# Kernel optimization log

Hardware: AMD Instinct MI355X
Metric: run time of the kernel (lower is better)

## Reference

```python
import jax, jax.numpy as jnp
import numpy as np

K = 3  # kernel_size per dim
DIM = 3
NUM_K = K ** DIM  # 27
# the 2^3 corner offsets of the linear B-spline support
OFFS = np.array([[(s >> d) & 1 for d in range(DIM)] for s in range(2 ** DIM)], dtype=np.int32)  # [8,3]
STRIDES = np.array([K ** d for d in range(DIM)], dtype=np.int32)  # [1,3,9]


def bspline_basis(pseudo):
    """Open B-spline basis, degree 1. pseudo: [E,3] in [0,1]. Returns basis [E,8], kidx [E,8]."""
    v = pseudo * (K - 1)
    i0 = jnp.clip(jnp.floor(v), 0, K - 2)
    f = v - i0  # fractional part in [0,1]
    i0 = i0.astype(jnp.int32)
    offs = jnp.asarray(OFFS)  # [8,3]
    w = jnp.where(offs[None].astype(bool), f[:, None, :], 1.0 - f[:, None, :])  # [E,8,3]
    basis = jnp.prod(w, axis=-1)  # [E,8]
    kidx = jnp.sum((i0[:, None, :] + offs[None]) * jnp.asarray(STRIDES)[None, None, :], axis=-1)  # [E,8]
    return basis, kidx


def spline_conv(x, src, dst, pseudo, W, Wroot, b, num_nodes):
    """SplineConv (degree 1, mean aggregation, root weight + bias)."""
    cout = W.shape[-1]
    xW = jnp.einsum('nc,kco->nko', x, W)  # [N,27,Cout]
    basis, kidx = bspline_basis(pseudo)
    flat = src[:, None] * NUM_K + kidx  # [E,8]
    g = xW.reshape(-1, cout)[flat]  # [E,8,Cout] -- dominant gather
    msg = jnp.einsum('es,eso->eo', basis, g)  # [E,Cout]
    agg = jax.ops.segment_sum(msg, dst, num_segments=num_nodes)
    cnt = jax.ops.segment_sum(jnp.ones((src.shape[0],), x.dtype), dst, num_segments=num_nodes)
    return agg / jnp.maximum(cnt, 1.0)[:, None] + x @ Wroot + b


def seg_max(x, seg, num_segments):
    m = jax.ops.segment_max(x, seg, num_segments=num_segments)
    return jnp.where(jnp.isfinite(m), m, 0.0)  # empty clusters -> 0


def setup_inputs() -> dict:
    key = jax.random.key(0)
    ks = jax.random.split(key, 16)
    N, E, B = 80000, 1280000, 16
    N1, N2 = N // 2, N1 if False else (N // 2) // 2  # N1=40000, N2=20000
    N1 = N // 2
    N2 = N1 // 2
    x = jax.random.normal(ks[0], (N, 2), dtype=jnp.float32)
    edge_index = jax.random.randint(ks[1], (2, E), 0, N, dtype=jnp.int32)
    edge_attr = jax.random.uniform(ks[2], (E, 3), dtype=jnp.float32)
    batch = jnp.sort(jax.random.randint(ks[3], (N,), 0, B, dtype=jnp.int32))
    cluster1 = jax.random.randint(ks[4], (N,), 0, N1, dtype=jnp.int32)
    cluster2 = jax.random.randint(ks[5], (N1,), 0, N2, dtype=jnp.int32)
    W1 = jax.random.normal(ks[6], (NUM_K, 2, 8), dtype=jnp.float32) * 0.3
    root1 = jax.random.normal(ks[7], (2, 8), dtype=jnp.float32) * 0.3
    b1 = jnp.zeros((8,), jnp.float32)
    W2 = jax.random.normal(ks[8], (NUM_K, 8, 16), dtype=jnp.float32) * 0.2
    root2 = jax.random.normal(ks[9], (8, 16), dtype=jnp.float32) * 0.2
    b2 = jnp.zeros((16,), jnp.float32)
    fc1_w = jax.random.normal(ks[10], (16, 64), dtype=jnp.float32) * 0.2
    fc1_b = jnp.zeros((64,), jnp.float32)
    fc2_w = jax.random.normal(ks[11], (64, 1), dtype=jnp.float32) * 0.2
    fc2_b = jnp.zeros((1,), jnp.float32)
    return dict(x=x, edge_index=edge_index, edge_attr=edge_attr, batch=batch,
                cluster1=cluster1, cluster2=cluster2,
                W1=W1, root1=root1, b1=b1, W2=W2, root2=root2, b2=b2,
                fc1_w=fc1_w, fc1_b=fc1_b, fc2_w=fc2_w, fc2_b=fc2_b)


def reference(x, edge_index, edge_attr, batch, cluster1, cluster2,
              W1, root1, b1, W2, root2, b2, fc1_w, fc1_b, fc2_w, fc2_b):
    N = x.shape[0]
    N1 = cluster1.max() * 0 + cluster2.shape[0]  # static: 40000
    N1 = cluster2.shape[0]
    N2 = N1 // 2
    B = 16
    src, dst = edge_index[0], edge_index[1]
    # level 1: SplineConv + ELU
    h = jax.nn.elu(spline_conv(x, src, dst, edge_attr, W1, root1, b1, N))
    # max_pool with precomputed cluster assignment (replaces graclus)
    x1 = seg_max(h, cluster1, N1)
    batch1 = jnp.maximum(jax.ops.segment_max(batch, cluster1, num_segments=N1), 0)
    src2 = cluster1[src]
    dst2 = cluster1[dst]
    # level 2: SplineConv + ELU on coarsened graph
    h2 = jax.nn.elu(spline_conv(x1, src2, dst2, edge_attr, W2, root2, b2, N1))
    x2 = seg_max(h2, cluster2, N2)
    batch2 = jnp.maximum(jax.ops.segment_max(batch1, cluster2, num_segments=N2), 0)
    # scatter_mean over graphs
    s = jax.ops.segment_sum(x2, batch2, num_segments=B)
    c = jax.ops.segment_sum(jnp.ones((N2,), x.dtype), batch2, num_segments=B)
    g = s / jnp.maximum(c, 1.0)[:, None]  # [B,16]
    g = jax.nn.elu(g @ fc1_w + fc1_b)  # dropout is identity in eval mode
    return jax.nn.elu(g @ fc2_w + fc2_b)  # [B,1]
```

## Files before the change

### kernel.cpp

```cpp
#include <hip/hip_runtime.h>
#include <hip/hip_fp16.h>
#include <math.h>


__device__ __forceinline__ float eluf(float x) {
    return x > 0.f ? x : (expf(x) - 1.f);
}

__device__ __forceinline__ float hlo(int v) {
    __half2 h; *(int*)&h = v; return __low2float(h);
}
__device__ __forceinline__ float hhi(int v) {
    __half2 h; *(int*)&h = v; return __high2float(h);
}

typedef _Float16 half2v __attribute__((ext_vector_type(2)));

__device__ __forceinline__ half2v uash2(unsigned u) {
    half2v h; *(unsigned*)&h = u; return h;
}

__device__ __forceinline__ float dot2f(half2v a, half2v b, float c) {
#if __has_builtin(__builtin_amdgcn_fdot2)
    return __builtin_amdgcn_fdot2(a, b, c, false);
#else
    return c + (float)a[0] * (float)b[0] + (float)a[1] * (float)b[1];
#endif
}

#define W1_STRIDE 20
#define W2H_STRIDE 68


__global__ __launch_bounds__(256) void hist_kernel(
    const int* __restrict__ ei, const int* __restrict__ cluster1,
    const int* __restrict__ cluster2,
    int* __restrict__ deg, int* __restrict__ rank,
    int* __restrict__ cdeg, int* __restrict__ rankC,
    int* __restrict__ c2deg, int* __restrict__ rank2,
    int E, int N, int N1)
{
    int i = blockIdx.x * 256 + threadIdx.x;
    if (i < E)  rank[i]  = atomicAdd(&deg[ei[E + i]], 1);
    if (i < N)  rankC[i] = atomicAdd(&cdeg[cluster1[i]], 1);
    if (i < N1) rank2[i] = atomicAdd(&c2deg[cluster2[i]], 1);
}

#define SCAN_CHUNK 4096

__global__ __launch_bounds__(256) void scan_a(
    const int* __restrict__ in0, int* __restrict__ out0, int* __restrict__ aux0, int L0, int nb0,
    const int* __restrict__ in1, int* __restrict__ out1, int* __restrict__ aux1, int L1, int nb1,
    const int* __restrict__ in2, int* __restrict__ out2, int* __restrict__ aux2, int L2)
{
    int b = blockIdx.x;
    const int* in; int* out; int* aux; int L;
    if (b < nb0)            { in = in0; out = out0; aux = aux0; L = L0; }
    else if (b < nb0 + nb1) { b -= nb0; in = in1; out = out1; aux = aux1; L = L1; }
    else                    { b -= nb0 + nb1; in = in2; out = out2; aux = aux2; L = L2; }

    __shared__ int ls[256];
    int t = threadIdx.x;
    int base = b * SCAN_CHUNK + t * 16;
    int v[16];
    int s = 0;
#pragma unroll
    for (int j = 0; j < 16; ++j) {
        int val = (base + j < L) ? in[base + j] : 0;
        v[j] = s;
        s += val;
    }
    ls[t] = s;
    __syncthreads();
    for (int off = 1; off < 256; off <<= 1) {
        int tv = (t >= off) ? ls[t - off] : 0;
        __syncthreads();
        ls[t] += tv;
        __syncthreads();
    }
    int excl = ls[t] - s;
#pragma unroll
    for (int j = 0; j < 16; ++j)
        if (base + j < L) out[base + j] = excl + v[j];
    if (t == 255) aux[b] = ls[255];
}

__global__ __launch_bounds__(64) void scan_b(
    int* __restrict__ aux0, int nb0, int* __restrict__ off0, int L0,
    int* __restrict__ aux1, int nb1, int* __restrict__ off1, int L1,
    int* __restrict__ aux2, int nb2, int* __restrict__ off2, int L2)
{
    if (threadIdx.x != 0) return;
    int* aux; int nb; int* off; int L;
    if (blockIdx.x == 0)      { aux = aux0; nb = nb0; off = off0; L = L0; }
    else if (blockIdx.x == 1) { aux = aux1; nb = nb1; off = off1; L = L1; }
    else                      { aux = aux2; nb = nb2; off = off2; L = L2; }
    int run = 0;
    for (int j = 0; j < nb; ++j) { int tv = aux[j]; aux[j] = run; run += tv; }
    off[L] = run;
}

__global__ __launch_bounds__(256) void scan_c(
    int* __restrict__ out0, const int* __restrict__ aux0, int L0, int nb0,
    int* __restrict__ out1, const int* __restrict__ aux1, int L1, int nb1,
    int* __restrict__ out2, const int* __restrict__ aux2, int L2)
{
    int b = blockIdx.x;
    int* out; const int* aux; int L;
    if (b < nb0)            { out = out0; aux = aux0; L = L0; }
    else if (b < nb0 + nb1) { b -= nb0; out = out1; aux = aux1; L = L1; }
    else                    { b -= nb0 + nb1; out = out2; aux = aux2; L = L2; }
    int add = aux[b];
    int base = b * SCAN_CHUNK + threadIdx.x * 16;
#pragma unroll
    for (int j = 0; j < 16; ++j)
        if (base + j < L) out[base + j] += add;
}

__global__ __launch_bounds__(256) void scatB_kernel(
    const int* __restrict__ ei, const float* __restrict__ attr,
    const int* __restrict__ cluster1, const int* __restrict__ cluster2,
    const float2* __restrict__ x, const float* __restrict__ W1,
    const int* __restrict__ doffs, const int* __restrict__ rank,
    const int* __restrict__ coff, const int* __restrict__ rankC,
    const int* __restrict__ c2off, const int* __restrict__ rank2,
    int* __restrict__ nidx, int* __restrict__ n1idx,
    int4* __restrict__ rec4, int E, int N, int N1)
{
    __shared__ float lw[27 * W1_STRIDE];
    for (int i = threadIdx.x; i < 27 * 16; i += 256)
        lw[(i >> 4) * W1_STRIDE + (i & 15)] = W1[i];
    __syncthreads();

    int i = blockIdx.x * 256 + threadIdx.x;
    if (i < E) {
        int s = ei[i], d = ei[E + i];
        int p = doffs[d] + rank[i];

        float vx = attr[3 * i] * 2.f, vy = attr[3 * i + 1] * 2.f, vz = attr[3 * i + 2] * 2.f;
        float ix = fmaxf(fminf(floorf(vx), 1.f), 0.f);
        float iy = fmaxf(fminf(floorf(vy), 1.f), 0.f);
        float iz = fmaxf(fminf(floorf(vz), 1.f), 0.f);
        float fx = vx - ix, fy = vy - iy, fz = vz - iz;
        int ibase = (int)ix + 3 * (int)iy + 9 * (int)iz;

        float2 xv = x[s];
        float wxv[2] = {1.f - fx, fx}, wyv[2] = {1.f - fy, fy}, wzv[2] = {1.f - fz, fz};
        float m[8];
#pragma unroll
        for (int o = 0; o < 8; ++o) m[o] = 0.f;
#pragma unroll
        for (int j = 0; j < 8; ++j) {
            int cx = j & 1, cy = (j >> 1) & 1, cz = j >> 2;
            float w = wxv[cx] * wyv[cy] * wzv[cz];
            const float* Wk = &lw[(ibase + cx + 3 * cy + 9 * cz) * W1_STRIDE];
            float a = w * xv.x, bb = w * xv.y;
            const float4 wa0 = *(const float4*)&Wk[0];
            const float4 wa1 = *(const float4*)&Wk[4];
            const float4 wb0 = *(const float4*)&Wk[8];
            const float4 wb1 = *(const float4*)&Wk[12];
            m[0] += a * wa0.x + bb * wb0.x;
            m[1] += a * wa0.y + bb * wb0.y;
            m[2] += a * wa0.z + bb * wb0.z;
            m[3] += a * wa0.w + bb * wb0.w;
            m[4] += a * wa1.x + bb * wb1.x;
            m[5] += a * wa1.y + bb * wb1.y;
            m[6] += a * wa1.z + bb * wb1.z;
            m[7] += a * wa1.w + bb * wb1.w;
        }

        unsigned hfx = __half_as_ushort(__float2half_rn(fx));
        unsigned hfy = __half_as_ushort(__float2half_rn(fy));
        unsigned hfz = __half_as_ushort(__float2half_rn(fz));
        int s2 = cluster1[s];
        int4 ra = make_int4(s2 | (ibase << 16),
                            (int)(hfx | (hfy << 16)), (int)hfz, d);
        __half2 h01 = __floats2half2_rn(m[0], m[1]);
        __half2 h23 = __floats2half2_rn(m[2], m[3]);
        __half2 h45 = __floats2half2_rn(m[4], m[5]);
        __half2 h67 = __floats2half2_rn(m[6], m[7]);
        int4 rb = make_int4(*(int*)&h01, *(int*)&h23, *(int*)&h45, *(int*)&h67);
        rec4[2 * (size_t)p]     = ra;
        rec4[2 * (size_t)p + 1] = rb;
    }
    if (i < N)  nidx[coff[cluster1[i]] + rankC[i]] = i;
    if (i < N1) n1idx[c2off[cluster2[i]] + rank2[i]] = i;
}

__global__ __launch_bounds__(256) void reduce1_kernel(
    const int* __restrict__ doffs, const unsigned short* __restrict__ recU,
    float* __restrict__ M1, int N)
{
    int lane = threadIdx.x & 63;
    int ch = lane & 7, q = lane >> 3;
    int d = (blockIdx.x << 2) + (threadIdx.x >> 6);
    if (d >= N) return;
    int beg = doffs[d], end = doffs[d + 1];
    float acc = 0.f;
    for (int p = beg + q; p < end; p += 8)
        acc += __half2float(__ushort_as_half(recU[(size_t)p * 16 + 8 + ch]));
    acc += __shfl_xor(acc, 8);
    acc += __shfl_xor(acc, 16);
    acc += __shfl_xor(acc, 32);
    if (q == 0)
        M1[(size_t)d * 8 + ch] = acc / fmaxf((float)(end - beg), 1.f);
}

__global__ __launch_bounds__(256) void node1_kernel(
    const int* __restrict__ coff, const int* __restrict__ nidx,
    const float* __restrict__ M1, const float2* __restrict__ x,
    const float* __restrict__ root1, const float* __restrict__ b1,
    const int* __restrict__ batch,
    float* __restrict__ x1c, unsigned short* __restrict__ x1chU,
    int* __restrict__ batch1, int N1)
{
    int t = blockIdx.x * 256 + threadIdx.x;
    if (t >= N1 * 8) return;
    int c = t >> 3, ch = t & 7;
    int cb = coff[c], ce = coff[c + 1];
    float r0 = root1[ch], r1 = root1[8 + ch], bo = b1[ch];
    float hm = -INFINITY;
    int bm = 0;
    for (int idx = cb; idx < ce; ++idx) {
        int d = nidx[idx];
        float2 xv = x[d];
        float h = eluf(M1[d * 8 + ch] + xv.x * r0 + xv.y * r1 + bo);
        hm = fmaxf(hm, h);
        bm = max(bm, batch[d]);
    }
    if (ce == cb) hm = 0.f;
    x1c[t] = hm;
    x1chU[t] = __half_as_ushort(__float2half_rn(hm));
    if (ch == 0) batch1[c] = bm;
}

__global__ __launch_bounds__(256) void edge2m_kernel(
    const int4* __restrict__ rec4, const unsigned short* __restrict__ x1chU,
    const float* __restrict__ W2, unsigned short* __restrict__ msg2h, int E)
{
    __shared__ unsigned lwh[27 * W2H_STRIDE];
    for (int i = threadIdx.x; i < 27 * 64; i += 256) {
        int k = i >> 6, r = i & 63;
        int o = r >> 2, c2 = r & 3;
        float a = W2[(k * 8 + 2 * c2) * 16 + o];
        float b = W2[(k * 8 + 2 * c2 + 1) * 16 + o];
        __half2 h = __floats2half2_rn(a, b);
        lwh[k * W2H_STRIDE + r] = *(unsigned*)&h;
    }
    __syncthreads();

    int t = blockIdx.x * 256 + threadIdx.x;
    if (t >= E * 4) return;
    int p = t >> 2, oq = t & 3;
    int4 m = rec4[2 * (size_t)p];
    int s2 = m.x & 0xFFFF;
    int ibase = (m.x >> 16) & 31;
    float fx = hlo(m.y), fy = hhi(m.y), fz = hlo(m.z);

    const uint4 xv4 = *(const uint4*)&x1chU[(size_t)s2 * 8];
    half2v xh0 = uash2(xv4.x), xh1 = uash2(xv4.y),
           xh2 = uash2(xv4.z), xh3 = uash2(xv4.w);

    float wx0 = 1.f - fx, wy0 = 1.f - fy, wz0 = 1.f - fz;
    float acc0 = 0.f, acc1 = 0.f, acc2 = 0.f, acc3 = 0.f;
#pragma unroll
    for (int j = 0; j < 8; ++j) {
        int cx = j & 1, cy = (j >> 1) & 1, cz = j >> 2;
        float w = (cx ? fx : wx0) * (cy ? fy : wy0) * (cz ? fz : wz0);
        int k = ibase + cx + 3 * cy + 9 * cz;
        const unsigned* base = &lwh[k * W2H_STRIDE + oq * 16];
        uint4 v0 = *(const uint4*)(base);
        uint4 v1 = *(const uint4*)(base + 4);
        uint4 v2 = *(const uint4*)(base + 8);
        uint4 v3 = *(const uint4*)(base + 12);
        float s0 = dot2f(xh0, uash2(v0.x), dot2f(xh1, uash2(v0.y),
                   dot2f(xh2, uash2(v0.z), dot2f(xh3, uash2(v0.w), 0.f))));
        float s1 = dot2f(xh0, uash2(v1.x), dot2f(xh1, uash2(v1.y),
                   dot2f(xh2, uash2(v1.z), dot2f(xh3, uash2(v1.w), 0.f))));
        float s2v = dot2f(xh0, uash2(v2.x), dot2f(xh1, uash2(v2.y),
                    dot2f(xh2, uash2(v2.z), dot2f(xh3, uash2(v2.w), 0.f))));
        float s3 = dot2f(xh0, uash2(v3.x), dot2f(xh1, uash2(v3.y),
                   dot2f(xh2, uash2(v3.z), dot2f(xh3, uash2(v3.w), 0.f))));
        acc0 = fmaf(w, s0, acc0);
        acc1 = fmaf(w, s1, acc1);
        acc2 = fmaf(w, s2v, acc2);
        acc3 = fmaf(w, s3, acc3);
    }
    __half2 lo = __floats2half2_rn(acc0, acc1);
    __half2 hi = __floats2half2_rn(acc2, acc3);
    uint2 outv = make_uint2(*(unsigned*)&lo, *(unsigned*)&hi);
    *(uint2*)&msg2h[(size_t)p * 16 + oq * 4] = outv;
}

__global__ __launch_bounds__(256) void reduce2_kernel(
    const int* __restrict__ coff, const int* __restrict__ nidx,
    const int* __restrict__ doffs, const unsigned short* __restrict__ msg2h,
    float* __restrict__ M2, int N1)
{
    int lane = threadIdx.x & 63;
    int o = lane & 15, q = lane >> 4;
    int c = (blockIdx.x << 2) + (threadIdx.x >> 6);
    if (c >= N1) return;
    int cb = coff[c], ce = coff[c + 1];
    float acc = 0.f;
    int cnt = 0;
    for (int idx = cb; idx < ce; ++idx) {
        int d = nidx[idx];
        int beg = doffs[d], end = doffs[d + 1];
        cnt += end - beg;
        for (int p = beg + q; p < end; p += 4)
            acc += __half2float(__ushort_as_half(msg2h[(size_t)p * 16 + o]));
    }
    acc += __shfl_xor(acc, 16);
    acc += __shfl_xor(acc, 32);
    if (q == 0) M2[(size_t)c * 16 + o] = acc / fmaxf((float)cnt, 1.f);
}

__global__ __launch_bounds__(256) void node2_kernel(
    const int* __restrict__ c2off, const int* __restrict__ n1idx,
    const float* __restrict__ M2, const float* __restrict__ x1c,
    const float* __restrict__ root2, const float* __restrict__ b2,
    const int* __restrict__ batch1,
    float* __restrict__ gsum, float* __restrict__ gcnt, int N2)
{
    __shared__ float ls[16 * 16];
    __shared__ float lc[16];
    for (int i = threadIdx.x; i < 256; i += 256) ls[i] = 0.f;
    if (threadIdx.x < 16) lc[threadIdx.x] = 0.f;
    __syncthreads();

    int c2 = blockIdx.x * 256 + threadIdx.x;
    if (c2 < N2) {
        int cb = c2off[c2], ce = c2off[c2 + 1];
        float hm[16];
#pragma unroll
        for (int o = 0; o < 16; ++o) hm[o] = -INFINITY;
        int bm = 0;
        for (int idx = cb; idx < ce; ++idx) {
            int n1 = n1idx[idx];
            const float4* xr4 = (const float4*)&x1c[(size_t)n1 * 8];
            float4 xa = xr4[0], xb = xr4[1];
            float xr[8] = {xa.x, xa.y, xa.z, xa.w, xb.x, xb.y, xb.z, xb.w};
#pragma unroll
            for (int o = 0; o < 16; ++o) {
                float v = M2[(size_t)n1 * 16 + o] + b2[o];
#pragma unroll
                for (int c8 = 0; c8 < 8; ++c8) v += xr[c8] * root2[c8 * 16 + o];
                hm[o] = fmaxf(hm[o], eluf(v));
            }
            bm = max(bm, batch1[n1]);
        }
        if (ce == cb) {
#pragma unroll
            for (int o = 0; o < 16; ++o) hm[o] = 0.f;
        }
#pragma unroll
        for (int o = 0; o < 16; ++o) atomicAdd(&ls[bm * 16 + o], hm[o]);
        atomicAdd(&lc[bm], 1.f);
    }
    __syncthreads();
    for (int i = threadIdx.x; i < 256; i += 256) unsafeAtomicAdd(&gsum[i], ls[i]);
    if (threadIdx.x < 16) unsafeAtomicAdd(&gcnt[threadIdx.x], lc[threadIdx.x]);
}

__global__ __launch_bounds__(256) void head_kernel(
    const float* __restrict__ gsum, const float* __restrict__ gcnt,
    const float* __restrict__ fc1_w, const float* __restrict__ fc1_b,
    const float* __restrict__ fc2_w, const float* __restrict__ fc2_b,
    float* __restrict__ out, int B)
{
    __shared__ float g[16 * 16];
    __shared__ float h1[16 * 64];
    int t = threadIdx.x;
    if (t < B * 16) {
        int b = t >> 4;
        g[t] = gsum[t] / fmaxf(gcnt[b], 1.f);
    }
    __syncthreads();
    for (int j = t; j < B * 64; j += 256) {
        int b = j >> 6, jj = j & 63;
        float s = fc1_b[jj];
#pragma unroll
        for (int c = 0; c < 16; ++c) s += g[b * 16 + c] * fc1_w[c * 64 + jj];
        h1[j] = eluf(s);
    }
    __syncthreads();
    if (t < B) {
        float s = fc2_b[0];
#pragma unroll
        for (int j = 0; j < 64; ++j) s += h1[t * 64 + j] * fc2_w[j];
        out[t] = eluf(s);
    }
}

extern "C" void kernel_launch(void* const* d_in, const int* in_sizes, int n_in,
                              void* d_out, int out_size, void* d_ws, size_t ws_size,
                              hipStream_t stream)
{
    const float* x        = (const float*)d_in[0];
    const int*   ei       = (const int*)  d_in[1];
    const float* attr     = (const float*)d_in[2];
    const int*   batch    = (const int*)  d_in[3];
    const int*   cluster1 = (const int*)  d_in[4];
    const int*   cluster2 = (const int*)  d_in[5];
    const float* W1       = (const float*)d_in[6];
    const float* root1    = (const float*)d_in[7];
    const float* b1       = (const float*)d_in[8];
    const float* W2       = (const float*)d_in[9];
    const float* root2    = (const float*)d_in[10];
    const float* b2       = (const float*)d_in[11];
    const float* fc1_w    = (const float*)d_in[12];
    const float* fc1_b    = (const float*)d_in[13];
    const float* fc2_w    = (const float*)d_in[14];
    const float* fc2_b    = (const float*)d_in[15];

    const int N  = in_sizes[0] / 2;
    const int E  = in_sizes[1] / 2;
    const int N1 = in_sizes[5];
    const int N2 = N1 / 2;
    const int B  = out_size;

    const int nb0 = (N  + SCAN_CHUNK - 1) / SCAN_CHUNK;
    const int nb1 = (N1 + SCAN_CHUNK - 1) / SCAN_CHUNK;
    const int nb2 = (N2 + SCAN_CHUNK - 1) / SCAN_CHUNK;

    int* wi = (int*)d_ws;
    size_t off = 0;
    auto alloc = [&](size_t n, size_t align = 1) {
        off = (off + align - 1) & ~(align - 1);
        size_t r = off; off += n; return r;
    };
    int*   deg    = wi + alloc(N);
    int*   cdeg   = wi + alloc(N1);
    int*   c2deg  = wi + alloc(N2);
    float* gsum   = (float*)(wi + alloc((size_t)B * 16));
    float* gcnt   = (float*)(wi + alloc(B));
    const size_t zcount = off;
    int*   doffs  = wi + alloc(N + 1);
    int*   coff   = wi + alloc(N1 + 1);
    int*   c2off  = wi + alloc(N2 + 1);
    int*   auxA   = wi + alloc(nb0);
    int*   auxB   = wi + alloc(nb1);
    int*   auxC   = wi + alloc(nb2);
    int*   rank   = wi + alloc(E);
    int*   rankC  = wi + alloc(N);
    int*   rank2  = wi + alloc(N1);
    int*   nidx   = wi + alloc(N);
    int*   n1idx  = wi + alloc(N1);
    int4*  rec4   = (int4*)(wi + alloc((size_t)E * 8, 8));
    unsigned short* msg2h = (unsigned short*)(wi + alloc((size_t)E * 8, 4));
    float* M1     = (float*)(wi + alloc((size_t)N * 8, 4));
    float* x1c    = (float*)(wi + alloc((size_t)N1 * 8, 4));
    unsigned short* x1chU = (unsigned short*)(wi + alloc((size_t)N1 * 4, 4));
    int*   batch1 = wi + alloc(N1);
    float* M2     = (float*)(wi + alloc((size_t)N1 * 16, 4));
    (void)ws_size;

    hipMemsetAsync(d_ws, 0, zcount * sizeof(int), stream);

    const int eb = (E + 255) / 256;
    hist_kernel<<<eb, 256, 0, stream>>>(ei, cluster1, cluster2,
                                        deg, rank, cdeg, rankC, c2deg, rank2, E, N, N1);
    scan_a<<<nb0 + nb1 + nb2, 256, 0, stream>>>(deg, doffs, auxA, N, nb0,
                                                cdeg, coff, auxB, N1, nb1,
                                                c2deg, c2off, auxC, N2);
    scan_b<<<3, 64, 0, stream>>>(auxA, nb0, doffs, N,
                                 auxB, nb1, coff, N1,
                                 auxC, nb2, c2off, N2);
    scan_c<<<nb0 + nb1 + nb2, 256, 0, stream>>>(doffs, auxA, N, nb0,
                                                coff, auxB, N1, nb1,
                                                c2off, auxC, N2);
    scatB_kernel<<<eb, 256, 0, stream>>>(ei, attr, cluster1, cluster2,
                                         (const float2*)x, W1,
                                         doffs, rank, coff, rankC, c2off, rank2,
                                         nidx, n1idx, rec4, E, N, N1);
    reduce1_kernel<<<(N + 3) / 4, 256, 0, stream>>>(
        doffs, (const unsigned short*)rec4, M1, N);
    node1_kernel<<<(N1 * 8 + 255) / 256, 256, 0, stream>>>(
        coff, nidx, M1, (const float2*)x, root1, b1, batch,
        x1c, x1chU, batch1, N1);
    edge2m_kernel<<<(E * 4 + 255) / 256, 256, 0, stream>>>(
        rec4, x1chU, W2, msg2h, E);
    reduce2_kernel<<<(N1 + 3) / 4, 256, 0, stream>>>(
        coff, nidx, doffs, msg2h, M2, N1);
    node2_kernel<<<(N2 + 255) / 256, 256, 0, stream>>>(
        c2off, n1idx, M2, x1c, root2, b2, batch1, gsum, gcnt, N2);
    head_kernel<<<1, 256, 0, stream>>>(gsum, gcnt, fc1_w, fc1_b, fc2_w, fc2_b,
                                       (float*)d_out, B);
}
```

Measured before the change: 350.2 us.

## Fuse scan passes into single-pass decoupled scan and merge reduce into node kernels

Replaces the three-kernel scan with one kernel in which each block publishes its total to a status array and spins on the totals of earlier blocks. It also fuses reduce1 into node1 and reduce2 into node2, so the per-node means M1 and M2 are computed on the fly and never written to memory. This removes four launches and the M1/M2 round trips. The cost is less parallelism: work becomes one wavefront per cluster walking its members serially, and node2 drops from one thread per cluster to one wavefront per cluster. The spin-wait assumes earlier blocks are resident or scheduled first.

```diff
diff --git a/kernel.cpp b/kernel.cpp
--- a/kernel.cpp
+++ b/kernel.cpp
@@ -48,18 +48,21 @@
 
 #define SCAN_CHUNK 4096
 
-__global__ __launch_bounds__(256) void scan_a(
-    const int* __restrict__ in0, int* __restrict__ out0, int* __restrict__ aux0, int L0, int nb0,
-    const int* __restrict__ in1, int* __restrict__ out1, int* __restrict__ aux1, int L1, int nb1,
-    const int* __restrict__ in2, int* __restrict__ out2, int* __restrict__ aux2, int L2)
+__global__ __launch_bounds__(256) void scan_one(
+    const int* __restrict__ in0, int* __restrict__ out0, int* __restrict__ st0, int L0, int nb0,
+    const int* __restrict__ in1, int* __restrict__ out1, int* __restrict__ st1, int L1, int nb1,
+    const int* __restrict__ in2, int* __restrict__ out2, int* __restrict__ st2, int L2)
 {
     int b = blockIdx.x;
-    const int* in; int* out; int* aux; int L;
-    if (b < nb0)            { in = in0; out = out0; aux = aux0; L = L0; }
-    else if (b < nb0 + nb1) { b -= nb0; in = in1; out = out1; aux = aux1; L = L1; }
-    else                    { b -= nb0 + nb1; in = in2; out = out2; aux = aux2; L = L2; }
+    const int* in; int* out; int* st; int L;
+    if (b < nb0)            { in = in0; out = out0; st = st0; L = L0; }
+    else if (b < nb0 + nb1) { b -= nb0; in = in1; out = out1; st = st1; L = L1; }
+    else                    { b -= nb0 + nb1; in = in2; out = out2; st = st2; L = L2; }
+    int nb = (L + SCAN_CHUNK - 1) / SCAN_CHUNK;
 
     __shared__ int ls[256];
+    __shared__ int pre[32];
+    __shared__ int blkExcl;
     int t = threadIdx.x;
     int base = b * SCAN_CHUNK + t * 16;
     int v[16];
@@ -79,42 +82,28 @@
         __syncthreads();
     }
     int excl = ls[t] - s;
+    int total = ls[255];
+    if (t == 255) {
+        __threadfence();
+        atomicExch(&st[b], total + 1);
+    }
+    if (t < b) {
+        int val;
+        do { val = atomicAdd(&st[t], 0); } while (val == 0);
+        pre[t] = val - 1;
+    }
+    __syncthreads();
+    if (t == 0) {
+        int r = 0;
+        for (int j = 0; j < b; ++j) r += pre[j];
+        blkExcl = r;
+    }
+    __syncthreads();
+    int be = blkExcl;
 #pragma unroll
     for (int j = 0; j < 16; ++j)
-        if (base + j < L) out[base + j] = excl + v[j];
-    if (t == 255) aux[b] = ls[255];
-}
-
-__global__ __launch_bounds__(64) void scan_b(
-    int* __restrict__ aux0, int nb0, int* __restrict__ off0, int L0,
-    int* __restrict__ aux1, int nb1, int* __restrict__ off1, int L1,
-    int* __restrict__ aux2, int nb2, int* __restrict__ off2, int L2)
-{
-    if (threadIdx.x != 0) return;
-    int* aux; int nb; int* off; int L;
-    if (blockIdx.x == 0)      { aux = aux0; nb = nb0; off = off0; L = L0; }
-    else if (blockIdx.x == 1) { aux = aux1; nb = nb1; off = off1; L = L1; }
-    else                      { aux = aux2; nb = nb2; off = off2; L = L2; }
-    int run = 0;
-    for (int j = 0; j < nb; ++j) { int tv = aux[j]; aux[j] = run; run += tv; }
-    off[L] = run;
-}
-
-__global__ __launch_bounds__(256) void scan_c(
-    int* __restrict__ out0, const int* __restrict__ aux0, int L0, int nb0,
-    int* __restrict__ out1, const int* __restrict__ aux1, int L1, int nb1,
-    int* __restrict__ out2, const int* __restrict__ aux2, int L2)
-{
-    int b = blockIdx.x;
-    int* out; const int* aux; int L;
-    if (b < nb0)            { out = out0; aux = aux0; L = L0; }
-    else if (b < nb0 + nb1) { b -= nb0; out = out1; aux = aux1; L = L1; }
-    else                    { b -= nb0 + nb1; out = out2; aux = aux2; L = L2; }
-    int add = aux[b];
-    int base = b * SCAN_CHUNK + threadIdx.x * 16;
-#pragma unroll
-    for (int j = 0; j < 16; ++j)
-        if (base + j < L) out[base + j] += add;
+        if (base + j < L) out[base + j] = be + excl + v[j];
+    if (b == nb - 1 && t == 255) out[L] = be + total;
 }
 
 __global__ __launch_bounds__(256) void scatB_kernel(
@@ -187,51 +176,44 @@
     if (i < N1) n1idx[c2off[cluster2[i]] + rank2[i]] = i;
 }
 
-__global__ __launch_bounds__(256) void reduce1_kernel(
+__global__ __launch_bounds__(256) void node1R_kernel(
+    const int* __restrict__ coff, const int* __restrict__ nidx,
     const int* __restrict__ doffs, const unsigned short* __restrict__ recU,
-    float* __restrict__ M1, int N)
-{
-    int lane = threadIdx.x & 63;
-    int ch = lane & 7, q = lane >> 3;
-    int d = (blockIdx.x << 2) + (threadIdx.x >> 6);
-    if (d >= N) return;
-    int beg = doffs[d], end = doffs[d + 1];
-    float acc = 0.f;
-    for (int p = beg + q; p < end; p += 8)
-        acc += __half2float(__ushort_as_half(recU[(size_t)p * 16 + 8 + ch]));
-    acc += __shfl_xor(acc, 8);
-    acc += __shfl_xor(acc, 16);
-    acc += __shfl_xor(acc, 32);
-    if (q == 0)
-        M1[(size_t)d * 8 + ch] = acc / fmaxf((float)(end - beg), 1.f);
-}
-
-__global__ __launch_bounds__(256) void node1_kernel(
-    const int* __restrict__ coff, const int* __restrict__ nidx,
-    const float* __restrict__ M1, const float2* __restrict__ x,
+    const float2* __restrict__ x,
     const float* __restrict__ root1, const float* __restrict__ b1,
     const int* __restrict__ batch,
     float* __restrict__ x1c, unsigned short* __restrict__ x1chU,
     int* __restrict__ batch1, int N1)
 {
-    int t = blockIdx.x * 256 + threadIdx.x;
-    if (t >= N1 * 8) return;
-    int c = t >> 3, ch = t & 7;
+    int lane = threadIdx.x & 63;
+    int ch = lane & 7, q = lane >> 3;
+    int c = (blockIdx.x << 2) + (threadIdx.x >> 6);
+    if (c >= N1) return;
     int cb = coff[c], ce = coff[c + 1];
     float r0 = root1[ch], r1 = root1[8 + ch], bo = b1[ch];
     float hm = -INFINITY;
     int bm = 0;
     for (int idx = cb; idx < ce; ++idx) {
         int d = nidx[idx];
+        int beg = doffs[d], end = doffs[d + 1];
+        float acc = 0.f;
+        for (int p = beg + q; p < end; p += 8)
+            acc += __half2float(__ushort_as_half(recU[(size_t)p * 16 + 8 + ch]));
+        acc += __shfl_xor(acc, 8);
+        acc += __shfl_xor(acc, 16);
+        acc += __shfl_xor(acc, 32);
+        float m1 = acc / fmaxf((float)(end - beg), 1.f);
         float2 xv = x[d];
-        float h = eluf(M1[d * 8 + ch] + xv.x * r0 + xv.y * r1 + bo);
+        float h = eluf(m1 + xv.x * r0 + xv.y * r1 + bo);
         hm = fmaxf(hm, h);
         bm = max(bm, batch[d]);
     }
     if (ce == cb) hm = 0.f;
-    x1c[t] = hm;
-    x1chU[t] = __half_as_ushort(__float2half_rn(hm));
-    if (ch == 0) batch1[c] = bm;
+    if (q == 0) {
+        x1c[(size_t)c * 8 + ch] = hm;
+        x1chU[(size_t)c * 8 + ch] = __half_as_ushort(__float2half_rn(hm));
+        if (ch == 0) batch1[c] = bm;
+    }
 }
 
 __global__ __launch_bounds__(256) void edge2m_kernel(
@@ -292,33 +274,11 @@
     *(uint2*)&msg2h[(size_t)p * 16 + oq * 4] = outv;
 }
 
-__global__ __launch_bounds__(256) void reduce2_kernel(
+__global__ __launch_bounds__(256) void node2R_kernel(
+    const int* __restrict__ c2off, const int* __restrict__ n1idx,
     const int* __restrict__ coff, const int* __restrict__ nidx,
     const int* __restrict__ doffs, const unsigned short* __restrict__ msg2h,
-    float* __restrict__ M2, int N1)
-{
-    int lane = threadIdx.x & 63;
-    int o = lane & 15, q = lane >> 4;
-    int c = (blockIdx.x << 2) + (threadIdx.x >> 6);
-    if (c >= N1) return;
-    int cb = coff[c], ce = coff[c + 1];
-    float acc = 0.f;
-    int cnt = 0;
-    for (int idx = cb; idx < ce; ++idx) {
-        int d = nidx[idx];
-        int beg = doffs[d], end = doffs[d + 1];
-        cnt += end - beg;
-        for (int p = beg + q; p < end; p += 4)
-            acc += __half2float(__ushort_as_half(msg2h[(size_t)p * 16 + o]));
-    }
-    acc += __shfl_xor(acc, 16);
-    acc += __shfl_xor(acc, 32);
-    if (q == 0) M2[(size_t)c * 16 + o] = acc / fmaxf((float)cnt, 1.f);
-}
-
-__global__ __launch_bounds__(256) void node2_kernel(
-    const int* __restrict__ c2off, const int* __restrict__ n1idx,
-    const float* __restrict__ M2, const float* __restrict__ x1c,
+    const float* __restrict__ x1c,
     const float* __restrict__ root2, const float* __restrict__ b2,
     const int* __restrict__ batch1,
     float* __restrict__ gsum, float* __restrict__ gcnt, int N2)
@@ -329,34 +289,45 @@
     if (threadIdx.x < 16) lc[threadIdx.x] = 0.f;
     __syncthreads();
 
-    int c2 = blockIdx.x * 256 + threadIdx.x;
+    int lane = threadIdx.x & 63;
+    int o = lane & 15, q = lane >> 4;
+    int c2 = (blockIdx.x << 2) + (threadIdx.x >> 6);
     if (c2 < N2) {
         int cb = c2off[c2], ce = c2off[c2 + 1];
-        float hm[16];
-#pragma unroll
-        for (int o = 0; o < 16; ++o) hm[o] = -INFINITY;
+        float r[8];
+#pragma unroll
+        for (int c8 = 0; c8 < 8; ++c8) r[c8] = root2[c8 * 16 + o];
+        float bo = b2[o];
+        float hmv = -INFINITY;
         int bm = 0;
         for (int idx = cb; idx < ce; ++idx) {
-            int n1 = n1idx[idx];
-            const float4* xr4 = (const float4*)&x1c[(size_t)n1 * 8];
+            int c1 = n1idx[idx];
+            int nb_ = coff[c1], ne_ = coff[c1 + 1];
+            float acc = 0.f;
+            int cnt = 0;
+            for (int j = nb_; j < ne_; ++j) {
+                int d = nidx[j];
+                int beg = doffs[d], end = doffs[d + 1];
+                cnt += end - beg;
+                for (int p = beg + q; p < end; p += 4)
+                    acc += __half2float(__ushort_as_half(msg2h[(size_t)p * 16 + o]));
+            }
+            acc += __shfl_xor(acc, 16);
+            acc += __shfl_xor(acc, 32);
+            float m2 = acc / fmaxf((float)cnt, 1.f);
+            const float4* xr4 = (const float4*)&x1c[(size_t)c1 * 8];
             float4 xa = xr4[0], xb = xr4[1];
-            float xr[8] = {xa.x, xa.y, xa.z, xa.w, xb.x, xb.y, xb.z, xb.w};
-#pragma unroll
-            for (int o = 0; o < 16; ++o) {
-                float v = M2[(size_t)n1 * 16 + o] + b2[o];
-#pragma unroll
-                for (int c8 = 0; c8 < 8; ++c8) v += xr[c8] * root2[c8 * 16 + o];
-                hm[o] = fmaxf(hm[o], eluf(v));
-            }
-            bm = max(bm, batch1[n1]);
+            float v = m2 + bo
+                    + xa.x * r[0] + xa.y * r[1] + xa.z * r[2] + xa.w * r[3]
+                    + xb.x * r[4] + xb.y * r[5] + xb.z * r[6] + xb.w * r[7];
+            hmv = fmaxf(hmv, eluf(v));
+            bm = max(bm, batch1[c1]);
         }
-        if (ce == cb) {
-#pragma unroll
-            for (int o = 0; o < 16; ++o) hm[o] = 0.f;
+        if (ce == cb) hmv = 0.f;
+        if (q == 0) {
+            atomicAdd(&ls[bm * 16 + o], hmv);
+            if (o == 0) atomicAdd(&lc[bm], 1.f);
         }
-#pragma unroll
-        for (int o = 0; o < 16; ++o) atomicAdd(&ls[bm * 16 + o], hm[o]);
-        atomicAdd(&lc[bm], 1.f);
     }
     __syncthreads();
     for (int i = threadIdx.x; i < 256; i += 256) unsafeAtomicAdd(&gsum[i], ls[i]);
@@ -435,13 +406,13 @@
     int*   c2deg  = wi + alloc(N2);
     float* gsum   = (float*)(wi + alloc((size_t)B * 16));
     float* gcnt   = (float*)(wi + alloc(B));
+    int*   st0    = wi + alloc(32);
+    int*   st1    = wi + alloc(32);
+    int*   st2    = wi + alloc(32);
     const size_t zcount = off;
     int*   doffs  = wi + alloc(N + 1);
     int*   coff   = wi + alloc(N1 + 1);
     int*   c2off  = wi + alloc(N2 + 1);
-    int*   auxA   = wi + alloc(nb0);
-    int*   auxB   = wi + alloc(nb1);
-    int*   auxC   = wi + alloc(nb2);
     int*   rank   = wi + alloc(E);
     int*   rankC  = wi + alloc(N);
     int*   rank2  = wi + alloc(N1);
@@ -449,11 +420,9 @@
     int*   n1idx  = wi + alloc(N1);
     int4*  rec4   = (int4*)(wi + alloc((size_t)E * 8, 8));
     unsigned short* msg2h = (unsigned short*)(wi + alloc((size_t)E * 8, 4));
-    float* M1     = (float*)(wi + alloc((size_t)N * 8, 4));
     float* x1c    = (float*)(wi + alloc((size_t)N1 * 8, 4));
     unsigned short* x1chU = (unsigned short*)(wi + alloc((size_t)N1 * 4, 4));
     int*   batch1 = wi + alloc(N1);
-    float* M2     = (float*)(wi + alloc((size_t)N1 * 16, 4));
     (void)ws_size;
 
     hipMemsetAsync(d_ws, 0, zcount * sizeof(int), stream);
@@ -461,30 +430,21 @@
     const int eb = (E + 255) / 256;
     hist_kernel<<<eb, 256, 0, stream>>>(ei, cluster1, cluster2,
                                         deg, rank, cdeg, rankC, c2deg, rank2, E, N, N1);
-    scan_a<<<nb0 + nb1 + nb2, 256, 0, stream>>>(deg, doffs, auxA, N, nb0,
-                                                cdeg, coff, auxB, N1, nb1,
-                                                c2deg, c2off, auxC, N2);
-    scan_b<<<3, 64, 0, stream>>>(auxA, nb0, doffs, N,
-                                 auxB, nb1, coff, N1,
-                                 auxC, nb2, c2off, N2);
-    scan_c<<<nb0 + nb1 + nb2, 256, 0, stream>>>(doffs, auxA, N, nb0,
-                                                coff, auxB, N1, nb1,
-                                                c2off, auxC, N2);
+    scan_one<<<nb0 + nb1 + nb2, 256, 0, stream>>>(deg, doffs, st0, N, nb0,
+                                                  cdeg, coff, st1, N1, nb1,
+                                                  c2deg, c2off, st2, N2);
     scatB_kernel<<<eb, 256, 0, stream>>>(ei, attr, cluster1, cluster2,
                                          (const float2*)x, W1,
                                          doffs, rank, coff, rankC, c2off, rank2,
                                          nidx, n1idx, rec4, E, N, N1);
-    reduce1_kernel<<<(N + 3) / 4, 256, 0, stream>>>(
-        doffs, (const unsigned short*)rec4, M1, N);
-    node1_kernel<<<(N1 * 8 + 255) / 256, 256, 0, stream>>>(
-        coff, nidx, M1, (const float2*)x, root1, b1, batch,
-        x1c, x1chU, batch1, N1);
+    node1R_kernel<<<(N1 + 3) / 4, 256, 0, stream>>>(
+        coff, nidx, doffs, (const unsigned short*)rec4, (const float2*)x,
+        root1, b1, batch, x1c, x1chU, batch1, N1);
     edge2m_kernel<<<(E * 4 + 255) / 256, 256, 0, stream>>>(
         rec4, x1chU, W2, msg2h, E);
-    reduce2_kernel<<<(N1 + 3) / 4, 256, 0, stream>>>(
-        coff, nidx, doffs, msg2h, M2, N1);
-    node2_kernel<<<(N2 + 255) / 256, 256, 0, stream>>>(
-        c2off, n1idx, M2, x1c, root2, b2, batch1, gsum, gcnt, N2);
+    node2R_kernel<<<(N2 + 3) / 4, 256, 0, stream>>>(
+        c2off, n1idx, coff, nidx, doffs, msg2h, x1c, root2, b2, batch1,
+        gsum, gcnt, N2);
     head_kernel<<<1, 256, 0, stream>>>(gsum, gcnt, fc1_w, fc1_b, fc2_w, fc2_b,
                                        (float*)d_out, B);
 }
```

New measurement: 427.9 us. 22.2% more time.
